# Optimization experiments

Hardware: AMD Instinct MI355X
Metric: run time of the kernel (lower is better)

Reference implementation:

```python
import jax, jax.numpy as jnp
import numpy as np

B, N, F_IN, F_HID, F_OUT = 16, 1024, 512, 512, 512


def setup_inputs() -> dict:
    key = jax.random.key(0)
    ks = jax.random.split(key, 8)
    return {
        "batch_graph": jax.random.normal(ks[0], (B, N, F_IN), dtype=jnp.float32),
        "adj": jax.random.uniform(ks[1], (B, N, N), dtype=jnp.float32),
        "W1": jax.random.normal(ks[2], (F_IN, F_HID), dtype=jnp.float32) * (1.0 / np.sqrt(F_IN)),
        "b1": jax.random.normal(ks[3], (F_HID,), dtype=jnp.float32) * 0.02,
        "W2": jax.random.normal(ks[4], (F_HID, F_HID), dtype=jnp.float32) * (1.0 / np.sqrt(F_HID)),
        "b2": jax.random.normal(ks[5], (F_HID,), dtype=jnp.float32) * 0.02,
        "W3": jax.random.normal(ks[6], (F_HID, F_OUT), dtype=jnp.float32) * (1.0 / np.sqrt(F_HID)),
        "b3": jax.random.normal(ks[7], (F_OUT,), dtype=jnp.float32) * 0.02,
    }


def _normalize_adj(adj):
    # torch: adj.sum(1) sums over rows -> per-column sums, shape [B, N]
    colsum = jnp.sum(adj, axis=1)
    r = jnp.where(colsum > 0, colsum ** -0.5, 0.0)  # inf -> 0 as in original
    # (adj @ diag(r)).T @ diag(r)  ==  r[:,None] * adj^T * r[None,:]  (per batch)
    return r[:, :, None] * jnp.swapaxes(adj, 1, 2) * r[:, None, :]


def reference(batch_graph, adj, W1, b1, W2, b2, W3, b3):
    # The original builds a dense (B*N)x(B*N) block-diagonal adjacency; the
    # block-diagonal matmul is mathematically a per-graph batched matmul.
    # Dropout is identity in eval mode.
    a = _normalize_adj(adj)  # [B, N, N]

    def layer(x, W, b):
        return jnp.einsum('bij,bjf->bif', a, x @ W) + b

    x = jax.nn.relu(layer(batch_graph, W1, b1))
    x = jax.nn.relu(layer(x, W2, b2))
    return layer(x, W3, b3)  # [B, N, F_OUT]
```

## Files before the change

kernel.cpp:

```cpp
#include <hip/hip_runtime.h>
#include <hip/hip_bf16.h>

typedef __bf16 bf16;
typedef __bf16 bf16x4 __attribute__((ext_vector_type(4)));
typedef __bf16 bf16x8 __attribute__((ext_vector_type(8)));
typedef float f32x4 __attribute__((ext_vector_type(4)));

#define B_ 16
#define N_ 1024
#define F_ 512

__device__ __forceinline__ float rdv(const void* p, size_t i, int f32) {
  return f32 ? ((const float*)p)[i] : (float)((const bf16*)p)[i];
}

__device__ __forceinline__ void gld16(const bf16* g, bf16* l) {
  __builtin_amdgcn_global_load_lds(
      (const __attribute__((address_space(1))) unsigned int*)g,
      (__attribute__((address_space(3))) unsigned int*)l, 16, 0, 0);
}

__global__ void k_detect(const unsigned* __restrict__ w, int* __restrict__ flag) {
  __shared__ int red[256];
  const int t = threadIdx.x;
  int c = 0;
  for (int i = t; i < 4096; i += 256) c += (((w[i] >> 7) & 0xFFu) >= 130u) ? 1 : 0;
  red[t] = c;
  __syncthreads();
  for (int s = 128; s > 0; s >>= 1) {
    if (t < s) red[t] += red[t + s];
    __syncthreads();
  }
  if (t == 0) flag[0] = (red[0] > 100) ? 1 : 0;
}

__global__ void k_prep(const void* b1, const void* b2, const void* b3,
                       const void* W1, const void* W2, const void* W3,
                       const void* X, const int* __restrict__ flag,
                       float* __restrict__ bc, bf16* __restrict__ Wt,
                       bf16* __restrict__ xc) {
  __shared__ float tile[32][33];
  const int bid = blockIdx.x;
  const int t = threadIdx.x;
  const int f = flag[0];
  if (bid < 6) {
    const int j = bid * 256 + t;
    const void* src = (j < 512) ? b1 : (j < 1024 ? b2 : b3);
    bc[j] = rdv(src, (size_t)(j & 511), f);
  } else if (bid < 774) {
    const int bid2 = bid - 6;
    const int z = bid2 >> 8, ti = bid2 & 255;
    const int f0 = (ti & 15) * 32, k0 = (ti >> 4) * 32;
    const int tx = t & 31, ty = t >> 5;
    const void* W = (z == 0) ? W1 : ((z == 1) ? W2 : W3);
    bf16* dst = Wt + (size_t)z * F_ * F_;
#pragma unroll
    for (int s = 0; s < 4; ++s)
      tile[ty + 8 * s][tx] = rdv(W, (size_t)(k0 + ty + 8 * s) * F_ + f0 + tx, f);
    __syncthreads();
#pragma unroll
    for (int s = 0; s < 4; ++s)
      dst[(size_t)(f0 + ty + 8 * s) * F_ + k0 + tx] = (bf16)tile[tx][ty + 8 * s];
  } else {
    const size_t i4 = ((size_t)(bid - 774) * 256 + t) * 4;
    if (f) {
      f32x4 v = *(const f32x4*)((const float*)X + i4);
      bf16 o[4] = {(bf16)v[0], (bf16)v[1], (bf16)v[2], (bf16)v[3]};
      *(ulong1*)&xc[i4] = *(ulong1*)o;
    } else {
      *(ulong1*)&xc[i4] = *(const ulong1*)((const bf16*)X + i4);
    }
  }
}

__global__ void k_colsum(const void* adj, const int* __restrict__ flag,
                         float* __restrict__ csp) {
  __shared__ float red[256];
  const int t = threadIdx.x;
  const int jj = t & 63, ic = t >> 6;
  const int b = blockIdx.y, z = blockIdx.z;
  const int j0 = blockIdx.x * 64;
  const size_t base = (size_t)b * N_ * N_ + (size_t)(z * 256 + ic * 64) * N_ + j0 + jj;
  float s = 0.f;
  if (flag[0]) {
    const float* p = (const float*)adj + base;
#pragma unroll 16
    for (int i = 0; i < 64; ++i) s += p[(size_t)i * N_];
  } else {
    const bf16* p = (const bf16*)adj + base;
#pragma unroll 16
    for (int i = 0; i < 64; ++i) s += (float)p[(size_t)i * N_];
  }
  red[t] = s;
  __syncthreads();
  if (t < 64)
    csp[((size_t)z * B_ + b) * N_ + j0 + t] = red[t] + red[t + 64] + red[t + 128] + red[t + 192];
}

__device__ __forceinline__ float csum(const float* csp, int b, int j) {
  float c = 0.f;
#pragma unroll
  for (int z = 0; z < 4; ++z) c += csp[((size_t)z * B_ + b) * N_ + j];
  return c;
}

__global__ void k_anorm(const void* adj, const int* __restrict__ flag,
                        const float* __restrict__ csp, bf16* __restrict__ anorm) {
  __shared__ float tile[64][65];
  __shared__ float rI[64], rJ[64];
  const int tx = threadIdx.x, ty = threadIdx.y;
  const int t = ty * 16 + tx;
  const int b = blockIdx.z, i0 = blockIdx.y * 64, j0 = blockIdx.x * 64;
  const size_t sb = (size_t)b * N_ * N_;
  if (t < 64) {
    float c = csum(csp, b, i0 + t);
    rI[t] = c > 0.f ? rsqrtf(c) : 0.f;
  } else if (t < 128) {
    float c = csum(csp, b, j0 + (t - 64));
    rJ[t - 64] = c > 0.f ? rsqrtf(c) : 0.f;
  }
  if (flag[0]) {
    const float* src = (const float*)adj + sb;
#pragma unroll
    for (int s = 0; s < 4; ++s) {
      const int jj = ty + 16 * s;
      f32x4 v = *(const f32x4*)&src[(size_t)(j0 + jj) * N_ + i0 + 4 * tx];
#pragma unroll
      for (int u = 0; u < 4; ++u) tile[jj][4 * tx + u] = v[u];
    }
  } else {
    const bf16* src = (const bf16*)adj + sb;
#pragma unroll
    for (int s = 0; s < 4; ++s) {
      const int jj = ty + 16 * s;
      bf16x4 v = *(const bf16x4*)&src[(size_t)(j0 + jj) * N_ + i0 + 4 * tx];
#pragma unroll
      for (int u = 0; u < 4; ++u) tile[jj][4 * tx + u] = (float)v[u];
    }
  }
  __syncthreads();
  bf16* dst = anorm + sb;
#pragma unroll
  for (int s = 0; s < 4; ++s) {
    const int ii = ty + 16 * s;
    const float ri = rI[ii];
    bf16x4 o;
#pragma unroll
    for (int u = 0; u < 4; ++u)
      o[u] = (bf16)(ri * tile[4 * tx + u][ii] * rJ[4 * tx + u]);
    *(bf16x4*)&dst[(size_t)(i0 + ii) * N_ + j0 + 4 * tx] = o;
  }
}

template <int BIAS, int RELU, int OUTDYN>
__global__ __launch_bounds__(256)
void k_gemm_bt(const bf16* __restrict__ A, const bf16* __restrict__ Bt,
               const float* __restrict__ bias, void* __restrict__ C,
               const int* __restrict__ flag,
               int Nc, int K, long sA, long sB, long sC) {
  __shared__ __align__(16) char smem[65536];
  const int tid = threadIdx.x;
  const int wid = tid >> 6, lane = tid & 63;
  const int wm = wid >> 1, wn = wid & 1;
  const int quad = lane >> 4, l16 = lane & 15;
  const int rl = lane >> 3;
  const int cg8 = ((lane & 7) ^ rl) * 8;
  const int h = l16 & 7;

  const bf16* gA = A + (size_t)blockIdx.z * sA + (size_t)blockIdx.y * 128 * K;
  const bf16* gB = Bt + (size_t)blockIdx.z * sB + (size_t)blockIdx.x * 128 * K;

  f32x4 acc[4][4];
#pragma unroll
  for (int i = 0; i < 4; ++i)
#pragma unroll
    for (int j = 0; j < 4; ++j) acc[i][j] = (f32x4){0.f, 0.f, 0.f, 0.f};

  auto stage = [&](int d, int k0) {
    bf16* As = (bf16*)(smem + d * 32768);
    bf16* Bs = (bf16*)(smem + d * 32768 + 16384);
#pragma unroll
    for (int i = 0; i < 4; ++i) {
      const int r0 = wid * 32 + i * 8;
      gld16(gA + (size_t)(r0 + rl) * K + k0 + cg8, &As[r0 * 64]);
      gld16(gB + (size_t)(r0 + rl) * K + k0 + cg8, &Bs[r0 * 64]);
    }
  };

  stage(0, 0);
  for (int k0 = 0; k0 < K; k0 += 64) {
    const int cur = (k0 >> 6) & 1;
    if (k0 + 64 < K) {
      stage(1 - cur, k0 + 64);
      asm volatile("s_waitcnt vmcnt(8)\n\ts_barrier" ::: "memory");
    } else {
      asm volatile("s_waitcnt vmcnt(0)\n\ts_barrier" ::: "memory");
    }
    const bf16* As = (const bf16*)(smem + cur * 32768);
    const bf16* Bs = (const bf16*)(smem + cur * 32768 + 16384);
#pragma unroll
    for (int s = 0; s < 2; ++s) {
      bf16x8 af[4], bfv[4];
#pragma unroll
      for (int tm = 0; tm < 4; ++tm)
        af[tm] = *(const bf16x8*)&As[(wm * 64 + tm * 16 + l16) * 64 +
                                     (((quad + 4 * s) ^ h) * 8)];
#pragma unroll
      for (int tn = 0; tn < 4; ++tn)
        bfv[tn] = *(const bf16x8*)&Bs[(wn * 64 + tn * 16 + l16) * 64 +
                                      (((quad + 4 * s) ^ h) * 8)];
#pragma unroll
      for (int tm = 0; tm < 4; ++tm)
#pragma unroll
        for (int tn = 0; tn < 4; ++tn)
          acc[tm][tn] =
              __builtin_amdgcn_mfma_f32_16x16x32_bf16(af[tm], bfv[tn], acc[tm][tn], 0, 0, 0);
    }
    asm volatile("s_barrier" ::: "memory");
  }

  const size_t cb = (size_t)blockIdx.z * sC;
  const int mb_w = blockIdx.y * 128 + wm * 64;
  const int nb_w = blockIdx.x * 128 + wn * 64;

  if (OUTDYN) {
    const int of32 = flag[0];
#pragma unroll
    for (int tn = 0; tn < 4; ++tn) {
      const int n = nb_w + tn * 16 + l16;
      float bv = BIAS ? bias[n] : 0.f;
#pragma unroll
      for (int tm = 0; tm < 4; ++tm) {
        const int m0 = mb_w + tm * 16 + quad * 4;
#pragma unroll
        for (int r = 0; r < 4; ++r) {
          float v = acc[tm][tn][r] + bv;
          if (RELU) v = v > 0.f ? v : 0.f;
          const size_t idx = cb + (size_t)(m0 + r) * Nc + n;
          if (of32) ((float*)C)[idx] = v;
          else      ((bf16*)C)[idx] = (bf16)v;
        }
      }
    }
  } else {
    bf16* W = (bf16*)smem + wid * (64 * 72);
#pragma unroll
    for (int tn = 0; tn < 4; ++tn) {
      const int n = nb_w + tn * 16 + l16;
      float bv = BIAS ? bias[n] : 0.f;
#pragma unroll
      for (int tm = 0; tm < 4; ++tm) {
#pragma unroll
        for (int r = 0; r < 4; ++r) {
          float v = acc[tm][tn][r] + bv;
          if (RELU) v = v > 0.f ? v : 0.f;
          W[(tm * 16 + quad * 4 + r) * 72 + tn * 16 + l16] = (bf16)v;
        }
      }
    }
    bf16* gC = (bf16*)C + cb;
#pragma unroll
    for (int i = 0; i < 8; ++i) {
      const int row = i * 8 + rl;
      bf16x8 v = *(const bf16x8*)&W[row * 72 + (lane & 7) * 8];
      *(bf16x8*)&gC[(size_t)(mb_w + row) * Nc + nb_w + (lane & 7) * 8] = v;
    }
  }
}

extern "C" void kernel_launch(void* const* d_in, const int* in_sizes, int n_in,
                              void* d_out, int out_size, void* d_ws, size_t ws_size,
                              hipStream_t stream) {
  char* ws = (char*)d_ws;
  float* csp  = (float*)ws;
  int*  flag  = (int*)(ws + 262144);
  float* bc   = (float*)(ws + 262400);
  bf16* anorm = (bf16*)(ws + 270592);
  bf16* Wt    = (bf16*)(ws + 270592 + 33554432);
  bf16* Zt    = (bf16*)(ws + 270592 + 33554432 + 3 * F_ * F_ * 2);
  bf16* Xc = (bf16*)d_out;

  const long sW = 0;
  const long sX = (long)N_ * F_;
  const long sZ = (long)F_ * N_;
  const long sAn = (long)N_ * N_;

  k_detect<<<1, 256, 0, stream>>>((const unsigned*)d_in[2], flag);
  k_prep<<<774 + (B_ * N_ * F_) / 1024, 256, 0, stream>>>(
      d_in[3], d_in[5], d_in[7], d_in[2], d_in[4], d_in[6], d_in[0], flag, bc, Wt, Xc);
  k_colsum<<<dim3(N_ / 64, B_, 4), 256, 0, stream>>>(d_in[1], flag, csp);
  k_anorm<<<dim3(N_ / 64, N_ / 64, B_), dim3(16, 16), 0, stream>>>(d_in[1], flag, csp, anorm);

  dim3 g1(N_ / 128, F_ / 128, B_);
  dim3 g2(F_ / 128, N_ / 128, B_);

  k_gemm_bt<0, 0, 0><<<g1, 256, 0, stream>>>(Wt,               Xc, nullptr,   Zt, flag, N_, F_, sW, sX, sZ);
  k_gemm_bt<1, 1, 0><<<g2, 256, 0, stream>>>(anorm,            Zt, bc,        Xc, flag, F_, N_, sAn, sZ, sX);
  k_gemm_bt<0, 0, 0><<<g1, 256, 0, stream>>>(Wt + F_ * F_,     Xc, nullptr,   Zt, flag, N_, F_, sW, sX, sZ);
  k_gemm_bt<1, 1, 0><<<g2, 256, 0, stream>>>(anorm,            Zt, bc + 512,  Xc, flag, F_, N_, sAn, sZ, sX);
  k_gemm_bt<0, 0, 0><<<g1, 256, 0, stream>>>(Wt + 2 * F_ * F_, Xc, nullptr,   Zt, flag, N_, F_, sW, sX, sZ);
  k_gemm_bt<1, 0, 1><<<g2, 256, 0, stream>>>(anorm,            Zt, bc + 1024, d_out, flag, F_, N_, sAn, sZ, sX);
}
```

Measured before the change: 296.2 us.

## Fuse column-sum into adjacency transpose and apply degree scaling in GEMM epilogues

Removes the separate column-sum pass over the adjacency by computing partial column sums inside the transpose kernel, which now writes an unscaled transposed bf16 adjacency. The D^-1/2 scaling is moved into the GEMM epilogues: the X·W GEMMs scale by r along the node dimension and the aggregation GEMMs scale rows by r, with r rebuilt from 16 partial sums per block. It also remaps the flat 1D grid so that each XCD handles two graphs, aiming for better L2 locality. This saves one full read of the large adjacency tensor, at the cost of a little extra epilogue work and a barrier in every GEMM.

Measured after the change: 259.6 us. 1.14x faster.

```diff
diff --git a/kernel.cpp b/kernel.cpp
--- a/kernel.cpp
+++ b/kernel.cpp
@@ -73,52 +73,14 @@
   }
 }
 
-__global__ void k_colsum(const void* adj, const int* __restrict__ flag,
-                         float* __restrict__ csp) {
-  __shared__ float red[256];
-  const int t = threadIdx.x;
-  const int jj = t & 63, ic = t >> 6;
-  const int b = blockIdx.y, z = blockIdx.z;
-  const int j0 = blockIdx.x * 64;
-  const size_t base = (size_t)b * N_ * N_ + (size_t)(z * 256 + ic * 64) * N_ + j0 + jj;
-  float s = 0.f;
-  if (flag[0]) {
-    const float* p = (const float*)adj + base;
-#pragma unroll 16
-    for (int i = 0; i < 64; ++i) s += p[(size_t)i * N_];
-  } else {
-    const bf16* p = (const bf16*)adj + base;
-#pragma unroll 16
-    for (int i = 0; i < 64; ++i) s += (float)p[(size_t)i * N_];
-  }
-  red[t] = s;
-  __syncthreads();
-  if (t < 64)
-    csp[((size_t)z * B_ + b) * N_ + j0 + t] = red[t] + red[t + 64] + red[t + 128] + red[t + 192];
-}
-
-__device__ __forceinline__ float csum(const float* csp, int b, int j) {
-  float c = 0.f;
-#pragma unroll
-  for (int z = 0; z < 4; ++z) c += csp[((size_t)z * B_ + b) * N_ + j];
-  return c;
-}
-
-__global__ void k_anorm(const void* adj, const int* __restrict__ flag,
-                        const float* __restrict__ csp, bf16* __restrict__ anorm) {
+__global__ void k_tran(const void* adj, const int* __restrict__ flag,
+                       bf16* __restrict__ adjT, float* __restrict__ csp) {
   __shared__ float tile[64][65];
-  __shared__ float rI[64], rJ[64];
+  __shared__ float red[4][64];
   const int tx = threadIdx.x, ty = threadIdx.y;
   const int t = ty * 16 + tx;
   const int b = blockIdx.z, i0 = blockIdx.y * 64, j0 = blockIdx.x * 64;
   const size_t sb = (size_t)b * N_ * N_;
-  if (t < 64) {
-    float c = csum(csp, b, i0 + t);
-    rI[t] = c > 0.f ? rsqrtf(c) : 0.f;
-  } else if (t < 128) {
-    float c = csum(csp, b, j0 + (t - 64));
-    rJ[t - 64] = c > 0.f ? rsqrtf(c) : 0.f;
-  }
   if (flag[0]) {
     const float* src = (const float*)adj + sb;
 #pragma unroll
@@ -139,26 +101,48 @@
     }
   }
   __syncthreads();
-  bf16* dst = anorm + sb;
+  {
+    const int cc = t & 63, g = t >> 6;
+    float s = 0.f;
+#pragma unroll
+    for (int r = 0; r < 16; ++r) s += tile[g * 16 + r][cc];
+    red[g][cc] = s;
+  }
+  bf16* dst = adjT + sb;
 #pragma unroll
   for (int s = 0; s < 4; ++s) {
     const int ii = ty + 16 * s;
-    const float ri = rI[ii];
     bf16x4 o;
 #pragma unroll
-    for (int u = 0; u < 4; ++u)
-      o[u] = (bf16)(ri * tile[4 * tx + u][ii] * rJ[4 * tx + u]);
+    for (int u = 0; u < 4; ++u) o[u] = (bf16)tile[4 * tx + u][ii];
     *(bf16x4*)&dst[(size_t)(i0 + ii) * N_ + j0 + 4 * tx] = o;
   }
-}
-
-template <int BIAS, int RELU, int OUTDYN>
+  __syncthreads();
+  if (t < 64)
+    csp[((size_t)(j0 >> 6) * B_ + b) * N_ + i0 + t] =
+        red[0][t] + red[1][t] + red[2][t] + red[3][t];
+}
+
+__device__ __forceinline__ float rscale(const float* __restrict__ csp, int b, int node) {
+  float c = 0.f;
+#pragma unroll
+  for (int z = 0; z < 16; ++z) c += csp[((size_t)z * B_ + b) * N_ + node];
+  return c > 0.f ? rsqrtf(c) : 0.f;
+}
+
+template <int BIAS, int RELU, int OUTDYN, int SCALEN, int SCALEM, int GX>
 __global__ __launch_bounds__(256)
 void k_gemm_bt(const bf16* __restrict__ A, const bf16* __restrict__ Bt,
                const float* __restrict__ bias, void* __restrict__ C,
-               const int* __restrict__ flag,
+               const int* __restrict__ flag, const float* __restrict__ csp,
                int Nc, int K, long sA, long sB, long sC) {
   __shared__ __align__(16) char smem[65536];
+  const int id = blockIdx.x;
+  const int xcd = id & 7, p = id >> 3;
+  const int bz = xcd * 2 + (p >> 5);
+  const int tl = p & 31;
+  const int bx = tl % GX, by = tl / GX;
+
   const int tid = threadIdx.x;
   const int wid = tid >> 6, lane = tid & 63;
   const int wm = wid >> 1, wn = wid & 1;
@@ -167,8 +151,8 @@
   const int cg8 = ((lane & 7) ^ rl) * 8;
   const int h = l16 & 7;
 
-  const bf16* gA = A + (size_t)blockIdx.z * sA + (size_t)blockIdx.y * 128 * K;
-  const bf16* gB = Bt + (size_t)blockIdx.z * sB + (size_t)blockIdx.x * 128 * K;
+  const bf16* gA = A + (size_t)bz * sA + (size_t)by * 128 * K;
+  const bf16* gB = Bt + (size_t)bz * sB + (size_t)bx * 128 * K;
 
   f32x4 acc[4][4];
 #pragma unroll
@@ -219,9 +203,18 @@
     asm volatile("s_barrier" ::: "memory");
   }
 
-  const size_t cb = (size_t)blockIdx.z * sC;
-  const int mb_w = blockIdx.y * 128 + wm * 64;
-  const int nb_w = blockIdx.x * 128 + wn * 64;
+  float* rsh = (float*)(smem + 37376);
+  if (SCALEN || SCALEM) {
+    if (tid < 128) {
+      const int node = (SCALEM ? by * 128 : bx * 128) + tid;
+      rsh[tid] = rscale(csp, bz, node);
+    }
+    __syncthreads();
+  }
+
+  const size_t cb = (size_t)bz * sC;
+  const int mb_w = by * 128 + wm * 64;
+  const int nb_w = bx * 128 + wn * 64;
 
   if (OUTDYN) {
     const int of32 = flag[0];
@@ -229,12 +222,16 @@
     for (int tn = 0; tn < 4; ++tn) {
       const int n = nb_w + tn * 16 + l16;
       float bv = BIAS ? bias[n] : 0.f;
+      const float cscale = SCALEN ? rsh[wn * 64 + tn * 16 + l16] : 1.f;
 #pragma unroll
       for (int tm = 0; tm < 4; ++tm) {
         const int m0 = mb_w + tm * 16 + quad * 4;
 #pragma unroll
         for (int r = 0; r < 4; ++r) {
-          float v = acc[tm][tn][r] + bv;
+          float v = acc[tm][tn][r];
+          if (SCALEM) v *= rsh[wm * 64 + tm * 16 + quad * 4 + r];
+          if (SCALEN) v *= cscale;
+          v += bv;
           if (RELU) v = v > 0.f ? v : 0.f;
           const size_t idx = cb + (size_t)(m0 + r) * Nc + n;
           if (of32) ((float*)C)[idx] = v;
@@ -248,11 +245,15 @@
     for (int tn = 0; tn < 4; ++tn) {
       const int n = nb_w + tn * 16 + l16;
       float bv = BIAS ? bias[n] : 0.f;
+      const float cscale = SCALEN ? rsh[wn * 64 + tn * 16 + l16] : 1.f;
 #pragma unroll
       for (int tm = 0; tm < 4; ++tm) {
 #pragma unroll
         for (int r = 0; r < 4; ++r) {
-          float v = acc[tm][tn][r] + bv;
+          float v = acc[tm][tn][r];
+          if (SCALEM) v *= rsh[wm * 64 + tm * 16 + quad * 4 + r];
+          if (SCALEN) v *= cscale;
+          v += bv;
           if (RELU) v = v > 0.f ? v : 0.f;
           W[(tm * 16 + quad * 4 + r) * 72 + tn * 16 + l16] = (bf16)v;
         }
@@ -273,11 +274,11 @@
                               hipStream_t stream) {
   char* ws = (char*)d_ws;
   float* csp  = (float*)ws;
-  int*  flag  = (int*)(ws + 262144);
-  float* bc   = (float*)(ws + 262400);
-  bf16* anorm = (bf16*)(ws + 270592);
-  bf16* Wt    = (bf16*)(ws + 270592 + 33554432);
-  bf16* Zt    = (bf16*)(ws + 270592 + 33554432 + 3 * F_ * F_ * 2);
+  int*  flag  = (int*)(ws + 1048576);
+  float* bc   = (float*)(ws + 1048832);
+  bf16* adjT  = (bf16*)(ws + 1056768);
+  bf16* Wt    = (bf16*)(ws + 1056768 + 33554432);
+  bf16* Zt    = (bf16*)(ws + 1056768 + 33554432 + 3 * F_ * F_ * 2);
   bf16* Xc = (bf16*)d_out;
 
   const long sW = 0;
@@ -288,16 +289,12 @@
   k_detect<<<1, 256, 0, stream>>>((const unsigned*)d_in[2], flag);
   k_prep<<<774 + (B_ * N_ * F_) / 1024, 256, 0, stream>>>(
       d_in[3], d_in[5], d_in[7], d_in[2], d_in[4], d_in[6], d_in[0], flag, bc, Wt, Xc);
-  k_colsum<<<dim3(N_ / 64, B_, 4), 256, 0, stream>>>(d_in[1], flag, csp);
-  k_anorm<<<dim3(N_ / 64, N_ / 64, B_), dim3(16, 16), 0, stream>>>(d_in[1], flag, csp, anorm);
-
-  dim3 g1(N_ / 128, F_ / 128, B_);
-  dim3 g2(F_ / 128, N_ / 128, B_);
-
-  k_gemm_bt<0, 0, 0><<<g1, 256, 0, stream>>>(Wt,               Xc, nullptr,   Zt, flag, N_, F_, sW, sX, sZ);
-  k_gemm_bt<1, 1, 0><<<g2, 256, 0, stream>>>(anorm,            Zt, bc,        Xc, flag, F_, N_, sAn, sZ, sX);
-  k_gemm_bt<0, 0, 0><<<g1, 256, 0, stream>>>(Wt + F_ * F_,     Xc, nullptr,   Zt, flag, N_, F_, sW, sX, sZ);
-  k_gemm_bt<1, 1, 0><<<g2, 256, 0, stream>>>(anorm,            Zt, bc + 512,  Xc, flag, F_, N_, sAn, sZ, sX);
-  k_gemm_bt<0, 0, 0><<<g1, 256, 0, stream>>>(Wt + 2 * F_ * F_, Xc, nullptr,   Zt, flag, N_, F_, sW, sX, sZ);
-  k_gemm_bt<1, 0, 1><<<g2, 256, 0, stream>>>(anorm,            Zt, bc + 1024, d_out, flag, F_, N_, sAn, sZ, sX);
-}
+  k_tran<<<dim3(N_ / 64, N_ / 64, B_), dim3(16, 16), 0, stream>>>(d_in[1], flag, adjT, csp);
+
+  k_gemm_bt<0, 0, 0, 1, 0, 8><<<512, 256, 0, stream>>>(Wt,               Xc, nullptr,   Zt, flag, csp, N_, F_, sW, sX, sZ);
+  k_gemm_bt<1, 1, 0, 0, 1, 4><<<512, 256, 0, stream>>>(adjT,             Zt, bc,        Xc, flag, csp, F_, N_, sAn, sZ, sX);
+  k_gemm_bt<0, 0, 0, 1, 0, 8><<<512, 256, 0, stream>>>(Wt + F_ * F_,     Xc, nullptr,   Zt, flag, csp, N_, F_, sW, sX, sZ);
+  k_gemm_bt<1, 1, 0, 0, 1, 4><<<512, 256, 0, stream>>>(adjT,             Zt, bc + 512,  Xc, flag, csp, F_, N_, sAn, sZ, sX);
+  k_gemm_bt<0, 0, 0, 1, 0, 8><<<512, 256, 0, stream>>>(Wt + 2 * F_ * F_, Xc, nullptr,   Zt, flag, csp, N_, F_, sW, sX, sZ);
+  k_gemm_bt<1, 0, 1, 0, 1, 4><<<512, 256, 0, stream>>>(adjT,             Zt, bc + 1024, d_out, flag, csp, F_, N_, sAn, sZ, sX);
+}
```
